# Kernel optimization log

Hardware: AMD Instinct MI355X
Metric: run time of the kernel (lower is better)

Reference implementation:

```python
import jax, jax.numpy as jnp
import numpy as np

D_MODEL = 1024
D_STATE = 64
D_CONV = 4
EXPAND = 2
HEADDIM = 128
D_INNER = EXPAND * D_MODEL      # 2048
NHEADS = D_INNER // HEADDIM     # 16
BATCH = 2
SEQLEN = 4096


def setup_inputs() -> dict:
    key = jax.random.key(0)
    ks = jax.random.split(key, 8)
    s = 0.02
    hidden_states = jax.random.normal(ks[0], (BATCH, SEQLEN, D_MODEL), jnp.float32)
    in_proj_w = jax.random.normal(ks[1], (2 * D_INNER, D_MODEL), jnp.float32) * s
    conv_w = jax.random.normal(ks[2], (D_INNER, 1, D_CONV), jnp.float32) * 0.2
    conv_b = jnp.zeros((D_INNER,), jnp.float32)
    dt_proj_w = jax.random.normal(ks[3], (NHEADS + 2 * D_STATE, D_INNER), jnp.float32) * s
    dt_proj_b = jnp.zeros((NHEADS + 2 * D_STATE,), jnp.float32)
    # dt_bias init as in module: inverse-softplus of dt ~ LogUniform(1e-3, 1e-1)
    dt = jnp.exp(jax.random.uniform(ks[4], (NHEADS,), jnp.float32)
                 * (np.log(0.1) - np.log(0.001)) + np.log(0.001))
    dt = jnp.clip(dt, 1e-4, None)
    dt_bias = dt + jnp.log(-jnp.expm1(-dt))
    # A_log = log(U(1,16)) so A = -exp(A_log) in [-16,-1] (stable decay)
    A_log = jnp.log(jax.random.uniform(ks[5], (D_INNER, D_STATE), jnp.float32) * 15.0 + 1.0)
    D = jnp.ones((D_INNER,), jnp.float32)
    norm_w = jnp.ones((D_INNER,), jnp.float32)
    norm_b = jnp.zeros((D_INNER,), jnp.float32)
    out_proj_w = jax.random.normal(ks[6], (D_MODEL, D_INNER), jnp.float32) * s
    return dict(hidden_states=hidden_states, in_proj_w=in_proj_w, conv_w=conv_w,
                conv_b=conv_b, dt_proj_w=dt_proj_w, dt_proj_b=dt_proj_b,
                dt_bias=dt_bias, A_log=A_log, D=D, norm_w=norm_w, norm_b=norm_b,
                out_proj_w=out_proj_w)


def reference(hidden_states, in_proj_w, conv_w, conv_b, dt_proj_w, dt_proj_b,
              dt_bias, A_log, D, norm_w, norm_b, out_proj_w):
    b, l, _ = hidden_states.shape
    # in_proj and split into x (SSM path) and z (gate)
    xz = hidden_states @ in_proj_w.T                      # (b,l,2*d_inner)
    x, z = jnp.split(xz, 2, axis=-1)                      # each (b,l,d_inner)
    # causal depthwise conv: torch pads both sides d_conv-1 then slices [:l]
    # == left-pad d_conv-1 valid conv
    xt = jnp.transpose(x, (0, 2, 1))                      # (b,d,l)
    xc = jax.lax.conv_general_dilated(
        xt, conv_w, window_strides=(1,), padding=[(D_CONV - 1, 0)],
        dimension_numbers=('NCH', 'OIH', 'NCH'),
        feature_group_count=D_INNER) + conv_b[None, :, None]
    u = jax.nn.silu(xc)                                   # (b,d,l)
    ub = jnp.transpose(u, (0, 2, 1))                      # (b,l,d)
    # dt/B/C projection from post-conv activations
    x_proj = ub @ dt_proj_w.T + dt_proj_b                 # (b,l,h+2n)
    dt = x_proj[..., :NHEADS]                             # (b,l,h)
    Bm = x_proj[..., NHEADS:NHEADS + D_STATE]             # (b,l,n)
    Cm = x_proj[..., NHEADS + D_STATE:]                   # (b,l,n)
    dt = jnp.repeat(dt, HEADDIM, axis=-1)                 # (b,l,d): head h -> (h p)
    dt = jax.nn.softplus(dt + jnp.repeat(dt_bias, HEADDIM)[None, None, :])
    A = -jnp.exp(A_log)                                   # (d,n)
    # selective scan, time-major to avoid materializing (b,d,l,n)
    u_l = jnp.transpose(ub, (1, 0, 2))                    # (l,b,d)
    dt_l = jnp.transpose(dt, (1, 0, 2))                   # (l,b,d)
    B_l = jnp.transpose(Bm, (1, 0, 2))                    # (l,b,n)
    C_l = jnp.transpose(Cm, (1, 0, 2))                    # (l,b,n)
    state0 = jnp.zeros((b, D_INNER, D_STATE), hidden_states.dtype)

    def step(state, inp):
        u_t, dt_t, B_t, C_t = inp
        dA = jnp.exp(dt_t[..., None] * A)                 # (b,d,n)
        state = state * dA + (dt_t * u_t)[..., None] * B_t[:, None, :]
        y_t = jnp.einsum('bdn,bn->bd', state, C_t)
        return state, y_t

    _, ys = jax.lax.scan(step, state0, (u_l, dt_l, B_l, C_l))  # ys (l,b,d)
    y = jnp.transpose(ys, (1, 0, 2)) + ub * D             # (b,l,d) skip term
    y = y * jax.nn.silu(z)                                # gate
    # LayerNorm over d_inner, eps=1e-5
    mu = jnp.mean(y, axis=-1, keepdims=True)
    var = jnp.var(y, axis=-1, keepdims=True)
    yn = (y - mu) / jnp.sqrt(var + 1e-5) * norm_w + norm_b
    return yn @ out_proj_w.T                              # (b,l,d_model)
```

## Files before the change

kernel.cpp:

```cpp
#include <hip/hip_runtime.h>
#include <hip/hip_bf16.h>

#define DMODEL 1024
#define DINNER 2048
#define DSTATE 64
#define BATCH 2
#define SEQLEN 4096
#define NROWS (BATCH*SEQLEN)
#define DTN 144
#define CHUNK 64
#define NCHUNK (SEQLEN/CHUNK)

typedef unsigned short u16;
typedef unsigned int u32;
typedef __attribute__((ext_vector_type(8))) short bf16x8;
typedef __attribute__((ext_vector_type(4))) float f32x4;
typedef __attribute__((ext_vector_type(4))) u32 u32x4;

__device__ __forceinline__ float b2f(u16 u){ u32 i = ((u32)u)<<16; return __builtin_bit_cast(float, i); }
__device__ __forceinline__ u16 f2b(float f){ u32 i = __builtin_bit_cast(u32, f); u32 r = (i + 0x7FFFu + ((i>>16)&1u))>>16; return (u16)r; }
__device__ __forceinline__ float silu_f(float x){ return x / (1.f + __expf(-x)); }
__device__ __forceinline__ float fexp2(float x){ float r; asm("v_exp_f32 %0, %1" : "=v"(r) : "v"(x)); return r; }

__device__ __forceinline__ void gload16(const u16* g, u16* l){
    __builtin_amdgcn_global_load_lds((const __attribute__((address_space(1))) void*)g,
                                     (__attribute__((address_space(3))) void*)l, 16, 0, 0);
}

__global__ __launch_bounds__(256) void cast_k(const float* __restrict__ in, u16* __restrict__ out, int n){
    int i = (blockIdx.x*256 + threadIdx.x)*8;
    if (i + 8 > n) return;
    f32x4 a = *(const f32x4*)(in + i);
    f32x4 b = *(const f32x4*)(in + i + 4);
    bf16x8 o;
    o[0]=(short)f2b(a[0]); o[1]=(short)f2b(a[1]); o[2]=(short)f2b(a[2]); o[3]=(short)f2b(a[3]);
    o[4]=(short)f2b(b[0]); o[5]=(short)f2b(b[1]); o[6]=(short)f2b(b[2]); o[7]=(short)f2b(b[3]);
    *(bf16x8*)(out + i) = o;
}

__global__ __launch_bounds__(256) void a2pack_k(const float* __restrict__ Alog, u32* __restrict__ A2v){
    int i = blockIdx.x*256 + threadIdx.x;
    int d = i & 2047, k4 = i >> 11;
    u32x4 o;
    #pragma unroll
    for (int j=0;j<4;++j){
        int n0 = (k4*4+j)*2;
        float a0 = -__expf(Alog[(long)d*64 + n0    ]) * 1.44269504f;
        float a1 = -__expf(Alog[(long)d*64 + n0 + 1]) * 1.44269504f;
        o[j] = (u32)f2b(a0) | ((u32)f2b(a1)<<16);
    }
    *(u32x4*)(A2v + ((long)k4*2048 + d)*4) = o;
}

__global__ __launch_bounds__(256) void a2packf_k(const float* __restrict__ Alog, float* __restrict__ A2f){
    int i = blockIdx.x*256 + threadIdx.x;
    int n = i >> 11, d = i & 2047;
    A2f[i] = -__expf(Alog[(long)d*64 + n]) * 1.44269504f;
}

__global__ __launch_bounds__(256) void xpinit_k(float* __restrict__ xpf, const float* __restrict__ bias){
    int i = blockIdx.x*256 + threadIdx.x;
    if (i >= NROWS*DTN) return;
    xpf[i] = bias[i % DTN];
}

__global__ __launch_bounds__(256) void gemmsk_k(
    const u16* __restrict__ A, const u16* __restrict__ B,
    float* __restrict__ Cf, int M, int N, int K, int klen)
{
    __shared__ u16 lA[64][72];
    __shared__ u16 lB[64][72];
    int tid = threadIdx.x;
    int bm = blockIdx.y, bn = blockIdx.x;
    int kbase = blockIdx.z * klen;
    int wave = tid>>6, lane = tid&63;
    int wr = wave>>1, wc = wave&1;
    f32x4 acc[2][2];
    #pragma unroll
    for (int r=0;r<2;++r)
    #pragma unroll
    for (int c=0;c<2;++c) acc[r][c] = 0.f;

    int lr = tid>>3;
    int lc = (tid&7)*8;
    long arow0 = (long)(bm*64 + lr)*K;
    long arow1 = (long)(bm*64 + lr + 32)*K;
    int brow0 = bn*64 + lr, brow1 = brow0 + 32;

    for (int k0 = kbase; k0 < kbase + klen; k0 += 64){
        __syncthreads();
        *(bf16x8*)&lA[lr][lc]    = *(const bf16x8*)(A + arow0 + k0 + lc);
        *(bf16x8*)&lA[lr+32][lc] = *(const bf16x8*)(A + arow1 + k0 + lc);
        bf16x8 b0 = 0, b1 = 0;
        if (brow0 < N) b0 = *(const bf16x8*)(B + (long)brow0*K + k0 + lc);
        if (brow1 < N) b1 = *(const bf16x8*)(B + (long)brow1*K + k0 + lc);
        *(bf16x8*)&lB[lr][lc]    = b0;
        *(bf16x8*)&lB[lr+32][lc] = b1;
        __syncthreads();
        int rA0 = wr*32 + (lane&15);
        int cB0 = wc*32 + (lane&15);
        int kl  = (lane>>4)*8;
        #pragma unroll
        for (int kk = 0; kk < 64; kk += 32){
            bf16x8 a0 = *(const bf16x8*)&lA[rA0   ][kk+kl];
            bf16x8 a1 = *(const bf16x8*)&lA[rA0+16][kk+kl];
            bf16x8 v0 = *(const bf16x8*)&lB[cB0   ][kk+kl];
            bf16x8 v1 = *(const bf16x8*)&lB[cB0+16][kk+kl];
            acc[0][0] = __builtin_amdgcn_mfma_f32_16x16x32_bf16(a0, v0, acc[0][0], 0,0,0);
            acc[0][1] = __builtin_amdgcn_mfma_f32_16x16x32_bf16(a0, v1, acc[0][1], 0,0,0);
            acc[1][0] = __builtin_amdgcn_mfma_f32_16x16x32_bf16(a1, v0, acc[1][0], 0,0,0);
            acc[1][1] = __builtin_amdgcn_mfma_f32_16x16x32_bf16(a1, v1, acc[1][1], 0,0,0);
        }
    }
    #pragma unroll
    for (int r=0;r<2;++r){
        #pragma unroll
        for (int c=0;c<2;++c){
            int col = bn*64 + wc*32 + c*16 + (lane&15);
            if (col >= N) continue;
            #pragma unroll
            for (int e=0;e<4;++e){
                int row = bm*64 + wr*32 + r*16 + (lane>>4)*4 + e;
                atomicAdd(&Cf[(long)row*N + col], acc[r][c][e]);
            }
        }
    }
}

__global__ __launch_bounds__(256) void gemm128_k(
    const u16* __restrict__ A, const u16* __restrict__ B,
    float* __restrict__ Cf, u16* __restrict__ Cb0, u16* __restrict__ Cb1, int split,
    int M, int N, int K)
{
    __shared__ u16 lA[128*64];
    __shared__ u16 lB[128*64];
    int tid = threadIdx.x, wave = tid>>6, lane = tid&63;
    int nwgx = gridDim.x;
    int flat = blockIdx.y*nwgx + blockIdx.x;
    int q = (nwgx*gridDim.y) >> 3;
    int nf = (flat & 7)*q + (flat >> 3);
    int bn = nf % nwgx, bm = nf / nwgx;
    int wr = wave>>1, wc = wave&1;
    f32x4 acc[4][4];
    #pragma unroll
    for (int i=0;i<4;++i)
    #pragma unroll
    for (int j=0;j<4;++j) acc[i][j] = 0.f;

    int srow = lane>>3;
    int scol = (lane&7)*8;
    const u16* Abase = A + (long)(bm*128)*K;
    const u16* Bbase = B + (long)(bn*128)*K;

    for (int k0 = 0; k0 < K; k0 += 64){
        __syncthreads();
        #pragma unroll
        for (int i=0;i<4;++i){
            int qq = i*4 + wave;
            int r = qq*8 + srow;
            gload16(Abase + (long)r*K + k0 + scol, &lA[qq*512]);
            gload16(Bbase + (long)r*K + k0 + scol, &lB[qq*512]);
        }
        __syncthreads();
        #pragma unroll
        for (int kk=0; kk<64; kk+=32){
            int kb = kk + ((lane>>4)<<3);
            bf16x8 af[4], bfr[4];
            #pragma unroll
            for (int i=0;i<4;++i) af[i]  = *(const bf16x8*)&lA[(wr*64 + i*16 + (lane&15))*64 + kb];
            #pragma unroll
            for (int j=0;j<4;++j) bfr[j] = *(const bf16x8*)&lB[(wc*64 + j*16 + (lane&15))*64 + kb];
            #pragma unroll
            for (int i=0;i<4;++i)
            #pragma unroll
            for (int j=0;j<4;++j)
                acc[i][j] = __builtin_amdgcn_mfma_f32_16x16x32_bf16(af[i], bfr[j], acc[i][j], 0,0,0);
        }
    }
    #pragma unroll
    for (int i=0;i<4;++i){
        #pragma unroll
        for (int j=0;j<4;++j){
            int col = bn*128 + wc*64 + j*16 + (lane&15);
            #pragma unroll
            for (int e=0;e<4;++e){
                int row = bm*128 + wr*64 + i*16 + (lane>>4)*4 + e;
                float v = acc[i][j][e];
                if (Cb0){
                    if (col < split) Cb0[(long)row*split + col] = f2b(v);
                    else             Cb1[(long)row*split + (col-split)] = f2b(v);
                } else {
                    Cf[(long)row*N + col] = v;
                }
            }
        }
    }
}

__global__ __launch_bounds__(256) void conv2_k(
    const u16* __restrict__ xb, const float* __restrict__ cw, const float* __restrict__ cb,
    u16* __restrict__ ub)
{
    int rb = blockIdx.x;
    int t0g = rb*8;
    int b = t0g >> 12, t0 = t0g & 4095;
    int d0 = threadIdx.x * 8;
    float w[4][8];
    #pragma unroll
    for (int e=0;e<8;++e){
        f32x4 wv = *(const f32x4*)(cw + (d0+e)*4);
        w[0][e]=wv[0]; w[1][e]=wv[1]; w[2][e]=wv[2]; w[3][e]=wv[3];
    }
    float bias[8];
    #pragma unroll
    for (int e=0;e<8;++e) bias[e] = cb[d0+e];

    bf16x8 xr[11];
    #pragma unroll
    for (int r=0;r<11;++r){
        int tr = t0 - 3 + r;
        bf16x8 v = 0;
        if (tr >= 0 && r < 8+3) v = *(const bf16x8*)(xb + ((long)(b*4096 + tr))*2048 + d0);
        xr[r] = v;
    }
    #pragma unroll
    for (int r=0;r<8;++r){
        bf16x8 o;
        #pragma unroll
        for (int e=0;e<8;++e){
            float acc = bias[e];
            #pragma unroll
            for (int j=0;j<4;++j) acc += b2f((u16)xr[r+j][e]) * w[j][e];
            o[e] = (short)f2b(silu_f(acc));
        }
        *(bf16x8*)(ub + ((long)(t0g + r))*2048 + d0) = o;
    }
}

__global__ __launch_bounds__(256) void dtv_k(const float* __restrict__ xp, const float* __restrict__ dtb, float* __restrict__ dtv){
    int i = blockIdx.x*256 + threadIdx.x;
    int row = i >> 4, h = i & 15;
    float x = xp[(long)row*DTN + h] + dtb[h];
    float sp = (x > 15.f) ? x : __logf(1.f + __expf(x));
    dtv[i] = sp;
}

__global__ __launch_bounds__(256) void scanA11_k(
    const u16* __restrict__ ub, const float* __restrict__ dtv,
    const float* __restrict__ xpf, const float* __restrict__ A2f,
    u16* __restrict__ states, float* __restrict__ dtsum)
{
    __shared__ u16 uL[CHUNK][256];
    int blk = blockIdx.x;
    int g2 = blk & 15; int g = g2 >> 1; int nh = g2 & 1;
    int bc = blk >> 4; int c = bc & (NCHUNK-1); int b = bc >> 6;
    int tid = threadIdx.x;
    int d = g*256 + tid;
    int n0 = nh*32;
    int base = b*SEQLEN + c*CHUNK;
    int h = __builtin_amdgcn_readfirstlane(g*2 + ((tid>>7)&1));

    for (int i = tid; i < CHUNK*32; i += 256){
        int t = i >> 5, seg = i & 31;
        *(bf16x8*)&uL[t][seg*8] = *(const bf16x8*)(ub + (long)(base+t)*2048 + g*256 + seg*8);
    }
    __syncthreads();

    float A2[32];
    #pragma unroll
    for (int j=0;j<32;++j) A2[j] = A2f[(long)(n0+j)*2048 + d];

    float s[32];
    #pragma unroll
    for (int n=0;n<32;++n) s[n] = 0.f;
    float dts = 0.f;
    #pragma unroll 2
    for (int t=0;t<CHUNK;++t){
        int row = __builtin_amdgcn_readfirstlane(base + t);
        const float* xr = xpf + (long)row*DTN + 16 + n0;
        float dtc = dtv[row*16 + h];
        float uu = b2f(uL[t][tid]);
        float dtu = dtc*uu;
        dts += dtc;
        #pragma unroll
        for (int n=0;n<32;++n){
            float e = fexp2(dtc*A2[n]);
            s[n] = fmaf(s[n], e, dtu*xr[n]);
        }
    }
    long sb = ((long)((b*NCHUNK + c)*64) + n0)*2048 + d;
    #pragma unroll
    for (int n=0;n<32;++n) states[sb + (long)n*2048] = f2b(s[n]);
    if (nh == 0) dtsum[(long)(b*NCHUNK+c)*2048 + d] = dts;
}

__global__ __launch_bounds__(256) void scanB8_k(
    u16* __restrict__ states, const float* __restrict__ dtsum, const u32* __restrict__ A2v)
{
    int idx = blockIdx.x*256 + threadIdx.x;
    int b = idx >> 17;
    int r = idx & 131071;
    int n = r >> 11; int d = r & 2047;
    u32 pk = A2v[((long)(n>>3)*2048 + d)*4 + ((n>>1)&3)];
    float A2 = (n&1) ? __builtin_bit_cast(float, pk & 0xFFFF0000u)
                     : __builtin_bit_cast(float, pk<<16);
    float carry = 0.f;
    for (int c=0;c<NCHUNK;++c){
        long off = ((long)((b*NCHUNK+c)*64 + n))*2048 + d;
        float loc = b2f(states[off]);
        states[off] = f2b(carry);
        float ds = dtsum[(long)(b*NCHUNK+c)*2048 + d];
        carry = carry*fexp2(A2*ds) + loc;
    }
}

__global__ __launch_bounds__(256) void scanC11_k(
    const u16* __restrict__ ub, const float* __restrict__ dtv,
    const float* __restrict__ xpf, const float* __restrict__ A2f,
    const u16* __restrict__ states, const float* __restrict__ Dv,
    u16* __restrict__ Y, int nh)
{
    __shared__ u16 uL[CHUNK][256];
    int blk = blockIdx.x;
    int g = blk & 7; int bc = blk >> 3; int c = bc & (NCHUNK-1); int b = bc >> 6;
    int tid = threadIdx.x;
    int d = g*256 + tid;
    int n0 = nh*32;
    int base = b*SEQLEN + c*CHUNK;
    int h = __builtin_amdgcn_readfirstlane(g*2 + ((tid>>7)&1));

    for (int i = tid; i < CHUNK*32; i += 256){
        int t = i >> 5, seg = i & 31;
        *(bf16x8*)&uL[t][seg*8] = *(const bf16x8*)(ub + (long)(base+t)*2048 + g*256 + seg*8);
    }
    __syncthreads();

    float A2[32];
    #pragma unroll
    for (int j=0;j<32;++j) A2[j] = A2f[(long)(n0+j)*2048 + d];

    float s[32];
    long sb = ((long)((b*NCHUNK + c)*64) + n0)*2048 + d;
    #pragma unroll
    for (int n=0;n<32;++n) s[n] = b2f(states[sb + (long)n*2048]);
    float Dd = Dv[d];
    for (int t=0;t<CHUNK;++t){
        int row = __builtin_amdgcn_readfirstlane(base + t);
        const float* xr = xpf + (long)row*DTN + 16 + n0;
        const float* xc = xr + 64;
        float dtc = dtv[row*16 + h];
        float uu = b2f(uL[t][tid]);
        float dtu = dtc*uu;
        float y0=0.f, y1=0.f;
        #pragma unroll
        for (int n=0;n<32;n+=2){
            float e0 = fexp2(dtc*A2[n]);
            float e1 = fexp2(dtc*A2[n+1]);
            s[n]   = fmaf(s[n],   e0, dtu*xr[n]);
            s[n+1] = fmaf(s[n+1], e1, dtu*xr[n+1]);
            y0 = fmaf(s[n],   xc[n],   y0);
            y1 = fmaf(s[n+1], xc[n+1], y1);
        }
        float y = y0 + y1;
        long yoff = (long)row*2048 + d;
        if (nh == 0){
            Y[yoff] = f2b(y);
        } else {
            y += b2f(Y[yoff]);
            Y[yoff] = f2b(fmaf(uu, Dd, y));
        }
    }
}

__global__ __launch_bounds__(256) void gatenorm_k(
    u16* __restrict__ Y, const u16* __restrict__ zb,
    const float* __restrict__ nw, const float* __restrict__ nb)
{
    int row = blockIdx.x;
    int tid = threadIdx.x;
    int d0 = tid*8;
    bf16x8 zv = *(const bf16x8*)(zb + (long)row*2048 + d0);
    bf16x8 yv = *(const bf16x8*)(Y + (long)row*2048 + d0);
    float gv[8];
    #pragma unroll
    for (int e=0;e<8;++e){
        float y = b2f((u16)yv[e]);
        float z = b2f((u16)zv[e]);
        gv[e] = y * silu_f(z);
    }
    float s1=0.f, s2=0.f;
    #pragma unroll
    for (int e=0;e<8;++e){ s1 += gv[e]; s2 += gv[e]*gv[e]; }
    #pragma unroll
    for (int o=32;o>0;o>>=1){ s1 += __shfl_xor(s1,o,64); s2 += __shfl_xor(s2,o,64); }
    __shared__ float red[2][4];
    int wave = tid>>6, lane = tid&63;
    if (lane==0){ red[0][wave]=s1; red[1][wave]=s2; }
    __syncthreads();
    s1 = red[0][0]+red[0][1]+red[0][2]+red[0][3];
    s2 = red[1][0]+red[1][1]+red[1][2]+red[1][3];
    float mu = s1 * (1.f/2048.f);
    float var = s2 * (1.f/2048.f) - mu*mu;
    float rs = rsqrtf(var + 1e-5f);
    bf16x8 o;
    #pragma unroll
    for (int e=0;e<8;++e){
        float v = (gv[e]-mu)*rs*nw[d0+e] + nb[d0+e];
        o[e] = (short)f2b(v);
    }
    *(bf16x8*)(Y + (long)row*2048 + d0) = o;
}

extern "C" void kernel_launch(void* const* d_in, const int* in_sizes, int n_in,
                              void* d_out, int out_size, void* d_ws, size_t ws_size,
                              hipStream_t stream)
{
    const float* hidden = (const float*)d_in[0];
    const float* w_in   = (const float*)d_in[1];
    const float* conv_w = (const float*)d_in[2];
    const float* conv_b = (const float*)d_in[3];
    const float* w_dt   = (const float*)d_in[4];
    const float* b_dt   = (const float*)d_in[5];
    const float* dt_bias= (const float*)d_in[6];
    const float* A_log  = (const float*)d_in[7];
    const float* Dv     = (const float*)d_in[8];
    const float* norm_w = (const float*)d_in[9];
    const float* norm_b = (const float*)d_in[10];
    const float* w_out  = (const float*)d_in[11];

    char* ws = (char*)d_ws;

    const size_t SZ_hb   = (size_t)NROWS*DMODEL*2;
    const size_t SZ_wib  = (size_t)2*DINNER*DMODEL*2;
    const size_t SZ_regA = SZ_hb + SZ_wib;
    const size_t SZ_big  = (size_t)NROWS*DINNER*2;
    const size_t SZ_wdtb = (size_t)DTN*DINNER*2;
    const size_t SZ_xpf  = (size_t)NROWS*DTN*4;
    const size_t SZ_dtv  = (size_t)NROWS*16*4;
    const size_t SZ_A2   = (size_t)DINNER*32*4;
    const size_t SZ_A2f  = (size_t)DINNER*DSTATE*4;
    const size_t SZ_states = (size_t)BATCH*NCHUNK*DSTATE*DINNER*2;
    const size_t SZ_dtsum  = (size_t)BATCH*NCHUNK*DINNER*4;

    size_t off = 0;
    auto take = [&](size_t bytes)->char*{ char* p = ws + off; off += (bytes + 255) & ~(size_t)255; return p; };

    char* regA = take(SZ_regA);
    u16*  hb   = (u16*)regA;
    u16*  wib  = (u16*)(regA + SZ_hb);
    u16*  wdtb = (u16*)regA;
    u16*  wob  = (u16*)(regA + ((SZ_wdtb + 255) & ~(size_t)255));
    u16*  xb   = (u16*)take(SZ_big);
    u16*  zb   = (u16*)take(SZ_big);
    u16*  ub   = (u16*)take(SZ_big);
    float* xpf = (float*)take(SZ_xpf);
    float* dtv = (float*)take(SZ_dtv);
    u32*  A2v  = (u32*)take(SZ_A2);
    float* A2f = (float*)take(SZ_A2f);
    u16*  states = (u16*)take(SZ_states);
    float* dtsum  = (float*)take(SZ_dtsum);
    u16*  Y    = xb;
    if (off > ws_size) return;

    { int n = NROWS*DMODEL;       cast_k<<<dim3((n/8+255)/256), dim3(256), 0, stream>>>(hidden, hb, n); }
    { int n = 2*DINNER*DMODEL;    cast_k<<<dim3((n/8+255)/256), dim3(256), 0, stream>>>(w_in, wib, n); }
    a2pack_k<<<dim3(DINNER*8/256), dim3(256), 0, stream>>>(A_log, A2v);
    a2packf_k<<<dim3(DINNER*DSTATE/256), dim3(256), 0, stream>>>(A_log, A2f);

    gemm128_k<<<dim3((2*DINNER)/128, NROWS/128), dim3(256), 0, stream>>>(hb, wib, nullptr, xb, zb, DINNER, NROWS, 2*DINNER, DMODEL);

    { int n = DTN*DINNER;         cast_k<<<dim3((n/8+255)/256), dim3(256), 0, stream>>>(w_dt, wdtb, n); }
    { int n = DMODEL*DINNER;      cast_k<<<dim3((n/8+255)/256), dim3(256), 0, stream>>>(w_out, wob, n); }

    conv2_k<<<dim3(NROWS/8), dim3(256), 0, stream>>>(xb, conv_w, conv_b, ub);
    xpinit_k<<<dim3((NROWS*DTN + 255)/256), dim3(256), 0, stream>>>(xpf, b_dt);
    gemmsk_k<<<dim3((DTN+63)/64, NROWS/64, 4), dim3(256), 0, stream>>>(ub, wdtb, xpf, NROWS, DTN, DINNER, DINNER/4);
    dtv_k<<<dim3(NROWS*16/256), dim3(256), 0, stream>>>(xpf, dt_bias, dtv);

    scanA11_k<<<dim3(BATCH*NCHUNK*16), dim3(256), 0, stream>>>(ub, dtv, xpf, A2f, states, dtsum);
    scanB8_k<<<dim3(BATCH*DSTATE*DINNER/256), dim3(256), 0, stream>>>(states, dtsum, A2v);
    scanC11_k<<<dim3(BATCH*NCHUNK*8), dim3(256), 0, stream>>>(ub, dtv, xpf, A2f, states, Dv, Y, 0);
    scanC11_k<<<dim3(BATCH*NCHUNK*8), dim3(256), 0, stream>>>(ub, dtv, xpf, A2f, states, Dv, Y, 1);

    gatenorm_k<<<dim3(NROWS), dim3(256), 0, stream>>>(Y, zb, norm_w, norm_b);
    gemm128_k<<<dim3(DMODEL/128, NROWS/128), dim3(256), 0, stream>>>(Y, wob, (float*)d_out, nullptr, nullptr, 0, NROWS, DMODEL, DINNER);
}
```

Measured before the change: 650.9 us.

## Merge state halves into 512-thread blocks in scan kernels and reduce via LDS

Both chunked scan passes now run the two 32-state halves as two 256-thread halves of a single 512-thread block instead of separate blocks or launches. In the output pass the two partial y sums are combined through a double-buffered shared array with a barrier each timestep. This drops the second scanC launch and the read-modify-write of Y in bf16, and it shares the uL staging load between halves. The cost is a per-timestep __syncthreads and larger blocks, which may lower occupancy.

```diff
diff --git a/kernel.cpp b/kernel.cpp
--- a/kernel.cpp
+++ b/kernel.cpp
@@ -245,22 +245,22 @@
     dtv[i] = sp;
 }
 
-__global__ __launch_bounds__(256) void scanA11_k(
+__global__ __launch_bounds__(512) void scanA12_k(
     const u16* __restrict__ ub, const float* __restrict__ dtv,
     const float* __restrict__ xpf, const float* __restrict__ A2f,
     u16* __restrict__ states, float* __restrict__ dtsum)
 {
     __shared__ u16 uL[CHUNK][256];
     int blk = blockIdx.x;
-    int g2 = blk & 15; int g = g2 >> 1; int nh = g2 & 1;
-    int bc = blk >> 4; int c = bc & (NCHUNK-1); int b = bc >> 6;
+    int g = blk & 7; int bc = blk >> 3; int c = bc & (NCHUNK-1); int b = bc >> 6;
     int tid = threadIdx.x;
-    int d = g*256 + tid;
-    int n0 = nh*32;
+    int half = tid >> 8, lt = tid & 255;
+    int d = g*256 + lt;
+    int n0 = half*32;
     int base = b*SEQLEN + c*CHUNK;
-    int h = __builtin_amdgcn_readfirstlane(g*2 + ((tid>>7)&1));
-
-    for (int i = tid; i < CHUNK*32; i += 256){
+    int h = __builtin_amdgcn_readfirstlane(g*2 + ((lt>>7)&1));
+
+    for (int i = tid; i < CHUNK*32; i += 512){
         int t = i >> 5, seg = i & 31;
         *(bf16x8*)&uL[t][seg*8] = *(const bf16x8*)(ub + (long)(base+t)*2048 + g*256 + seg*8);
     }
@@ -279,7 +279,7 @@
         int row = __builtin_amdgcn_readfirstlane(base + t);
         const float* xr = xpf + (long)row*DTN + 16 + n0;
         float dtc = dtv[row*16 + h];
-        float uu = b2f(uL[t][tid]);
+        float uu = b2f(uL[t][lt]);
         float dtu = dtc*uu;
         dts += dtc;
         #pragma unroll
@@ -291,7 +291,7 @@
     long sb = ((long)((b*NCHUNK + c)*64) + n0)*2048 + d;
     #pragma unroll
     for (int n=0;n<32;++n) states[sb + (long)n*2048] = f2b(s[n]);
-    if (nh == 0) dtsum[(long)(b*NCHUNK+c)*2048 + d] = dts;
+    if (half == 0) dtsum[(long)(b*NCHUNK+c)*2048 + d] = dts;
 }
 
 __global__ __launch_bounds__(256) void scanB8_k(
@@ -314,22 +314,24 @@
     }
 }
 
-__global__ __launch_bounds__(256) void scanC11_k(
+__global__ __launch_bounds__(512) void scanC13_k(
     const u16* __restrict__ ub, const float* __restrict__ dtv,
     const float* __restrict__ xpf, const float* __restrict__ A2f,
     const u16* __restrict__ states, const float* __restrict__ Dv,
-    u16* __restrict__ Y, int nh)
+    u16* __restrict__ Y)
 {
     __shared__ u16 uL[CHUNK][256];
+    __shared__ float yl[2][256];
     int blk = blockIdx.x;
     int g = blk & 7; int bc = blk >> 3; int c = bc & (NCHUNK-1); int b = bc >> 6;
     int tid = threadIdx.x;
-    int d = g*256 + tid;
-    int n0 = nh*32;
+    int half = tid >> 8, lt = tid & 255;
+    int d = g*256 + lt;
+    int n0 = half*32;
     int base = b*SEQLEN + c*CHUNK;
-    int h = __builtin_amdgcn_readfirstlane(g*2 + ((tid>>7)&1));
-
-    for (int i = tid; i < CHUNK*32; i += 256){
+    int h = __builtin_amdgcn_readfirstlane(g*2 + ((lt>>7)&1));
+
+    for (int i = tid; i < CHUNK*32; i += 512){
         int t = i >> 5, seg = i & 31;
         *(bf16x8*)&uL[t][seg*8] = *(const bf16x8*)(ub + (long)(base+t)*2048 + g*256 + seg*8);
     }
@@ -349,7 +351,7 @@
         const float* xr = xpf + (long)row*DTN + 16 + n0;
         const float* xc = xr + 64;
         float dtc = dtv[row*16 + h];
-        float uu = b2f(uL[t][tid]);
+        float uu = b2f(uL[t][lt]);
         float dtu = dtc*uu;
         float y0=0.f, y1=0.f;
         #pragma unroll
@@ -361,14 +363,12 @@
             y0 = fmaf(s[n],   xc[n],   y0);
             y1 = fmaf(s[n+1], xc[n+1], y1);
         }
-        float y = y0 + y1;
-        long yoff = (long)row*2048 + d;
-        if (nh == 0){
-            Y[yoff] = f2b(y);
-        } else {
-            y += b2f(Y[yoff]);
-            Y[yoff] = f2b(fmaf(uu, Dd, y));
-        }
+        float yh = y0 + y1;
+        int p = t & 1;
+        if (half) yl[p][lt] = yh;
+        __syncthreads();
+        if (!half)
+            Y[(long)row*2048 + d] = f2b(fmaf(uu, Dd, yh + yl[p][lt]));
     }
 }
 
@@ -477,10 +477,9 @@
     gemmsk_k<<<dim3((DTN+63)/64, NROWS/64, 4), dim3(256), 0, stream>>>(ub, wdtb, xpf, NROWS, DTN, DINNER, DINNER/4);
     dtv_k<<<dim3(NROWS*16/256), dim3(256), 0, stream>>>(xpf, dt_bias, dtv);
 
-    scanA11_k<<<dim3(BATCH*NCHUNK*16), dim3(256), 0, stream>>>(ub, dtv, xpf, A2f, states, dtsum);
+    scanA12_k<<<dim3(BATCH*NCHUNK*8), dim3(512), 0, stream>>>(ub, dtv, xpf, A2f, states, dtsum);
     scanB8_k<<<dim3(BATCH*DSTATE*DINNER/256), dim3(256), 0, stream>>>(states, dtsum, A2v);
-    scanC11_k<<<dim3(BATCH*NCHUNK*8), dim3(256), 0, stream>>>(ub, dtv, xpf, A2f, states, Dv, Y, 0);
-    scanC11_k<<<dim3(BATCH*NCHUNK*8), dim3(256), 0, stream>>>(ub, dtv, xpf, A2f, states, Dv, Y, 1);
+    scanC13_k<<<dim3(BATCH*NCHUNK*8), dim3(512), 0, stream>>>(ub, dtv, xpf, A2f, states, Dv, Y);
 
     gatenorm_k<<<dim3(NROWS), dim3(256), 0, stream>>>(Y, zb, norm_w, norm_b);
     gemm128_k<<<dim3(DMODEL/128, NROWS/128), dim3(256), 0, stream>>>(Y, wob, (float*)d_out, nullptr, nullptr, 0, NROWS, DMODEL, DINNER);
```

After: 827.5 us. 27.1% more time.
